# Performance work log

Measured on AMD Instinct MI355X. Metric: run time of the kernel, lower is better.

Reference implementation:

```python
import jax, jax.numpy as jnp
import numpy as np

B, N, D, H, L = 32, 576, 768, 8, 2
HD = D // H            # head_dim = 96
MLP = 4 * D            # 3072
GRID = 24              # sqrt(576), == max_positions
MP = 24                # max_positions
SD = 64                # spatial_dim
EPS = 1e-5


def _ln(x, g, b):
    m = jnp.mean(x, axis=-1, keepdims=True)
    v = jnp.mean((x - m) ** 2, axis=-1, keepdims=True)
    return (x - m) * jax.lax.rsqrt(v + EPS) * g + b


def setup_inputs() -> dict:
    key = jax.random.key(0)
    ks = jax.random.split(key, 16)
    s = 0.02
    inp = {
        "x": jax.random.normal(ks[0], (B, N, D), jnp.float32),
        # spatial position encoding params
        "row_embed": jax.random.normal(ks[1], (MP, SD // 2), jnp.float32) * s,
        "col_embed": jax.random.normal(ks[2], (MP, SD // 2), jnp.float32) * s,
        "pos_w": jax.random.normal(ks[3], (SD, D), jnp.float32) * s,
        "pos_b": jnp.zeros((D,), jnp.float32),
        "rel_bias": jax.random.normal(ks[4], (2 * MP - 1, 2 * MP - 1), jnp.float32) * s,
        # per-layer params, stacked on leading L axis
        "ln1_g": jnp.ones((L, D), jnp.float32),
        "ln1_b": jnp.zeros((L, D), jnp.float32),
        "ln2_g": jnp.ones((L, D), jnp.float32),
        "ln2_b": jnp.zeros((L, D), jnp.float32),
        "Wq": jax.random.normal(ks[5], (L, D, D), jnp.float32) * s,
        "bq": jnp.zeros((L, D), jnp.float32),
        "Wk": jax.random.normal(ks[6], (L, D, D), jnp.float32) * s,
        "bk": jnp.zeros((L, D), jnp.float32),
        "Wv": jax.random.normal(ks[7], (L, D, D), jnp.float32) * s,
        "bv": jnp.zeros((L, D), jnp.float32),
        "Wo": jax.random.normal(ks[8], (L, D, D), jnp.float32) * s,
        "bo": jnp.zeros((L, D), jnp.float32),
        "W1": jax.random.normal(ks[9], (L, D, MLP), jnp.float32) * s,
        "b1": jnp.zeros((L, MLP), jnp.float32),
        "W2": jax.random.normal(ks[10], (L, MLP, D), jnp.float32) * s,
        "b2": jnp.zeros((L, D), jnp.float32),
    }
    return inp


def reference(x, row_embed, col_embed, pos_w, pos_b, rel_bias,
              ln1_g, ln1_b, ln2_g, ln2_b,
              Wq, bq, Wk, bk, Wv, bv, Wo, bo,
              W1, b1, W2, b2):
    scale = HD ** -0.5

    # ---- absolute 2D position encoding (N = GRID*GRID, no CLS) ----
    pe = jnp.concatenate([
        jnp.broadcast_to(row_embed[:, None, :], (GRID, GRID, SD // 2)),
        jnp.broadcast_to(col_embed[None, :, :], (GRID, GRID, SD // 2)),
    ], axis=-1).reshape(N, SD)                      # [N, SD]
    x = x + (pe @ pos_w + pos_b)                    # broadcast over B

    # ---- relative position bias [N, N] ----
    coords = jnp.stack(jnp.meshgrid(jnp.arange(GRID), jnp.arange(GRID),
                                    indexing="ij")).reshape(2, N)  # [2, N]
    rel = coords[:, :, None] - coords[:, None, :]   # [2, N, N]
    idx = (rel[0] + MP - 1) * (2 * MP - 1) + (rel[1] + MP - 1)
    bias = rel_bias.reshape(-1)[idx]                # [N, N]

    # ---- reasoning layers ----
    for l in range(L):
        n1 = _ln(x, ln1_g[l], ln1_b[l])
        q = (n1 @ Wq[l] + bq[l]).reshape(B, N, H, HD)
        k = (n1 @ Wk[l] + bk[l]).reshape(B, N, H, HD)
        v = (n1 @ Wv[l] + bv[l]).reshape(B, N, H, HD)
        scores = jnp.einsum("bnhd,bmhd->bhnm", q, k) * scale + bias
        attn = jax.nn.softmax(scores, axis=-1)
        out = jnp.einsum("bhnm,bmhd->bnhd", attn, v).reshape(B, N, D)
        x = x + (out @ Wo[l] + bo[l])
        n2 = _ln(x, ln2_g[l], ln2_b[l])
        h = jax.nn.gelu(n2 @ W1[l] + b1[l], approximate=False)
        x = x + (h @ W2[l] + b2[l])
    return x
```

## Files before the change

kernel.cpp:

```cpp
#include <hip/hip_runtime.h>
#include <hip/hip_bf16.h>
#include <cstdint>
#include <cstddef>

typedef unsigned short u16;
using frag  = __attribute__((ext_vector_type(8))) short;
using f32x4 = __attribute__((ext_vector_type(4))) float;

#define DEV __device__ __forceinline__

DEV float bf2f(u16 u) { union { unsigned int i; float f; } x; x.i = ((unsigned int)u) << 16; return x.f; }
DEV u16 f2bf(float f) {
  union { float f; unsigned int i; } x; x.f = f;
  unsigned int r = x.i + 0x7fffu + ((x.i >> 16) & 1u);
  return (u16)(r >> 16);
}

#define MFMA16(a, b, c) __builtin_amdgcn_mfma_f32_16x16x32_bf16((a), (b), (c), 0, 0, 0)

DEV void cp16_g2l(const u16* g, u16* l) {
  __builtin_amdgcn_global_load_lds(
      reinterpret_cast<const __attribute__((address_space(1))) unsigned int*>(
          reinterpret_cast<uintptr_t>(g)),
      reinterpret_cast<__attribute__((address_space(3))) unsigned int*>(
          reinterpret_cast<uintptr_t>(l)),
      16, 0, 0);
}

template<int N> DEV void waitvm() {
  if constexpr (N == 0)      asm volatile("s_waitcnt vmcnt(0)" ::: "memory");
  else if constexpr (N == 3) asm volatile("s_waitcnt vmcnt(3)" ::: "memory");
  else if constexpr (N == 4) asm volatile("s_waitcnt vmcnt(4)" ::: "memory");
  else if constexpr (N == 6) asm volatile("s_waitcnt vmcnt(6)" ::: "memory");
  else if constexpr (N == 8) asm volatile("s_waitcnt vmcnt(8)" ::: "memory");
}

DEV void phase_barrier() {
  asm volatile("" ::: "memory");
  __builtin_amdgcn_sched_barrier(0);
  __builtin_amdgcn_s_barrier();
  __builtin_amdgcn_sched_barrier(0);
  asm volatile("" ::: "memory");
}

#define SB   32
#define SN   576
#define SD_  768
#define SH   8
#define SHD  96
#define SMLP 3072
#define BN_  (SB * SN)
#define IMG  (SN * SD_)
#define QKVS 2304

#define P_RE   0
#define P_CE   768
#define P_PW   1536
#define P_PB   50688
#define P_REL  51456
#define P_L1G  53696
#define P_L1B  55232
#define P_L2G  56768
#define P_L2B  58304
#define P_BQ   59840
#define P_BK   61376
#define P_BV   62912
#define P_BO   64448
#define P_B1   65984
#define P_B2   72128
#define P_FQB  73664
#define P_TOT  78272

__global__ void detect_kernel(const void* probe, int* flag) {
  if (threadIdx.x == 0 && blockIdx.x == 0) {
    unsigned int w = *(const unsigned int*)probe;
    flag[0] = (w == 0x3F800000u) ? 1 : 0;
  }
}

__global__ void canon_params(const void* re, const void* ce, const void* pw, const void* pb,
                             const void* rel, const void* l1g, const void* l1b,
                             const void* l2g, const void* l2b,
                             const void* pbq, const void* pbk, const void* pbv, const void* pbo,
                             const void* pb1, const void* pb2,
                             u16* __restrict__ P, const int* __restrict__ flag) {
  int i = blockIdx.x * 256 + threadIdx.x;
  const void* src; int si;
  if      (i < 768)     { src = re;  si = i; }
  else if (i < 1536)    { src = ce;  si = i - 768; }
  else if (i < 50688)   { src = pw;  si = i - 1536; }
  else if (i < 51456)   { src = pb;  si = i - 50688; }
  else if (i < 53665)   { src = rel; si = i - 51456; }
  else if (i < P_L1G)   { return; }
  else if (i < P_L1B)   { src = l1g; si = i - P_L1G; }
  else if (i < P_L2G)   { src = l1b; si = i - P_L1B; }
  else if (i < P_L2B)   { src = l2g; si = i - P_L2G; }
  else if (i < P_BQ)    { src = l2b; si = i - P_L2B; }
  else if (i < P_BK)    { src = pbq; si = i - P_BQ; }
  else if (i < P_BV)    { src = pbk; si = i - P_BK; }
  else if (i < P_BO)    { src = pbv; si = i - P_BV; }
  else if (i < P_B1)    { src = pbo; si = i - P_BO; }
  else if (i < P_B2)    { src = pb1; si = i - P_B1; }
  else if (i < P_FQB)   { src = pb2; si = i - P_B2; }
  else if (i < P_TOT) {
    int j = i - P_FQB, l = j / 2304, c = j % 2304;
    src = (c < 768) ? pbq : (c < 1536 ? pbk : pbv);
    si = l * 768 + (c % 768);
  }
  else return;
  P[i] = flag[0] ? f2bf(((const float*)src)[si]) : ((const u16*)src)[si];
}

__global__ void posenc_kernel(const u16* __restrict__ P, float* __restrict__ pe) {
  int n = blockIdx.x;
  int r = n / 24, c = n % 24;
  const u16* re = P + P_RE;
  const u16* ce = P + P_CE;
  const u16* pw = P + P_PW;
  const u16* pb = P + P_PB;
  for (int d = threadIdx.x; d < SD_; d += 256) {
    float acc = bf2f(pb[d]);
    for (int s = 0; s < 32; ++s) {
      acc += bf2f(re[r * 32 + s]) * bf2f(pw[s * SD_ + d]);
      acc += bf2f(ce[c * 32 + s]) * bf2f(pw[(32 + s) * SD_ + d]);
    }
    pe[n * SD_ + d] = acc;
  }
}

__global__ void bias_kernel(const u16* __restrict__ P, float* __restrict__ biasT) {
  int i = blockIdx.x * 256 + threadIdx.x;
  if (i < SN * SN) {
    int qi = i / SN, kj = i % SN;
    int ri = qi / 24, ci = qi % 24, rj = kj / 24, cj = kj % 24;
    int idx = (ri - rj + 23) * 47 + (ci - cj + 23);
    biasT[i] = bf2f(P[P_REL + idx]);
  }
}

__global__ void xinit_kernel(const void* __restrict__ xin, const float* __restrict__ pe,
                             float* __restrict__ X, const int* __restrict__ flag) {
  int idx = (blockIdx.x * 256 + threadIdx.x) * 4;
  int b = blockIdx.y;
  float vx, vy, vz, vw;
  if (flag[0]) {
    float4 t = *(const float4*)((const float*)xin + (size_t)b * IMG + idx);
    vx = t.x; vy = t.y; vz = t.z; vw = t.w;
  } else {
    ushort4 t = *(const ushort4*)((const u16*)xin + (size_t)b * IMG + idx);
    vx = bf2f(t.x); vy = bf2f(t.y); vz = bf2f(t.z); vw = bf2f(t.w);
  }
  float4 p = *(const float4*)(pe + idx);
  float4 o;
  o.x = vx + p.x; o.y = vy + p.y; o.z = vz + p.z; o.w = vw + p.w;
  *(float4*)(X + (size_t)b * IMG + idx) = o;
}

__global__ void transpose_any(const void* __restrict__ W, size_t eOff,
                              u16* __restrict__ Wt, int K, int N,
                              const int* __restrict__ flag) {
  __shared__ u16 tile[64][65];
  const int fp32 = flag[0];
  int n0 = blockIdx.x * 64, k0 = blockIdx.y * 64;
  int tx = threadIdx.x, ty = threadIdx.y;
#pragma unroll
  for (int j = 0; j < 16; ++j) {
    int k = ty + 4 * j;
    size_t si = eOff + (size_t)(k0 + k) * N + n0 + tx;
    tile[k][tx] = fp32 ? f2bf(((const float*)W)[si]) : ((const u16*)W)[si];
  }
  __syncthreads();
#pragma unroll
  for (int j = 0; j < 16; ++j) {
    int n = ty + 4 * j;
    Wt[(size_t)(n0 + n) * K + k0 + tx] = tile[tx][n];
  }
}

__global__ __launch_bounds__(256) void ln_kernel(const float* __restrict__ X,
                                                 const u16* __restrict__ g,
                                                 const u16* __restrict__ bb,
                                                 u16* __restrict__ Outn) {
  int row = blockIdx.x * 4 + (threadIdx.x >> 6);
  int lane = threadIdx.x & 63;
  const float* xr = X + (size_t)row * SD_;
  float4 v[3];
  float s = 0.f, sq = 0.f;
#pragma unroll
  for (int i = 0; i < 3; ++i) {
    v[i] = *(const float4*)(xr + i * 256 + lane * 4);
    s += v[i].x + v[i].y + v[i].z + v[i].w;
    sq += v[i].x * v[i].x + v[i].y * v[i].y + v[i].z * v[i].z + v[i].w * v[i].w;
  }
#pragma unroll
  for (int o = 1; o < 64; o <<= 1) {
    s += __shfl_xor(s, o, 64);
    sq += __shfl_xor(sq, o, 64);
  }
  float mean = s * (1.0f / 768.0f);
  float var = sq * (1.0f / 768.0f) - mean * mean;
  float rstd = rsqrtf(fmaxf(var, 0.f) + 1e-5f);
  u16* orow = Outn + (size_t)row * SD_;
#pragma unroll
  for (int i = 0; i < 3; ++i) {
    int d = i * 256 + lane * 4;
    ushort4 gv = *(const ushort4*)(g + d);
    ushort4 bv = *(const ushort4*)(bb + d);
    ushort4 ov;
    ov.x = f2bf((v[i].x - mean) * rstd * bf2f(gv.x) + bf2f(bv.x));
    ov.y = f2bf((v[i].y - mean) * rstd * bf2f(gv.y) + bf2f(bv.y));
    ov.z = f2bf((v[i].z - mean) * rstd * bf2f(gv.z) + bf2f(bv.z));
    ov.w = f2bf((v[i].w - mean) * rstd * bf2f(gv.w) + bf2f(bv.w));
    *(ushort4*)(orow + d) = ov;
  }
}

template<int MREP, int MODE>
__global__ __launch_bounds__(512, 2) void gemm256(
    const u16* __restrict__ A, const u16* __restrict__ Bt,
    const u16* __restrict__ bias, u16* __restrict__ Out,
    float* __restrict__ Xres, int Ncols, int K) {
  constexpr int BM = MREP * 32;
  constexpr int ASLOT = BM * 32;
  constexpr int BSLOT = 256 * 32;
  constexpr int LPT = (BM == 256) ? 4 : 3;
  __shared__ __align__(1024) u16 sA[4 * ASLOT];
  __shared__ __align__(1024) u16 sB[4 * BSLOT];

  const int tid = threadIdx.x;
  const int lane = tid & 63;
  const int w = tid >> 6;
  const int wm = w >> 2, wn = w & 3;
  const int m16 = lane & 15, q4 = lane >> 4;
  const int bn = blockIdx.x, bm = blockIdx.y;
  const int nt = K >> 5;

  const int srow = tid >> 2;
  const int kcol = (((tid & 3) ^ ((tid >> 3) & 3)) << 3);
  const u16* Ag = A + (size_t)(bm * BM + srow) * K + kcol;
  const u16* Bg = Bt + (size_t)(bn * 256 + srow) * K + kcol;
  const size_t rstep = (size_t)128 * K;
  u16* const Adst = sA + tid * 8;
  u16* const Bdst = sB + tid * 8;

  const int xk = ((q4 ^ ((m16 >> 1) & 3)) << 4);
  const char* const aBase = (const char*)sA + (((wm * (BM / 2) + m16) << 6) + xk);
  const char* const bBase = (const char*)sB + (((wn * 64 + m16) << 6) + xk);

  f32x4 acc[MREP][4] = {};

  auto stage_a = [&](int t) {
    const int s = t & 3;
    cp16_g2l(Ag + (size_t)t * 32, Adst + s * ASLOT);
    if constexpr (BM == 256) cp16_g2l(Ag + (size_t)t * 32 + rstep, Adst + s * ASLOT + 4096);
  };
  auto stage_b = [&](int t) {
    const int s = t & 3;
    cp16_g2l(Bg + (size_t)t * 32, Bdst + s * BSLOT);
    cp16_g2l(Bg + (size_t)t * 32 + rstep, Bdst + s * BSLOT + 4096);
  };

  if (nt > 0) { stage_a(0); stage_b(0); }
  if (nt > 1) { stage_a(1); stage_b(1); }
  if (nt > 2) { stage_a(2); stage_b(2); }
  if (nt > 2) waitvm<2 * LPT>(); else waitvm<0>();
  phase_barrier();

  for (int t = 0; t < nt; ++t) {
    const int s = t & 3;
    const bool st = (t + 3) < nt;
    const char* const aS = aBase + s * (ASLOT * 2);
    const char* const bS = bBase + s * (BSLOT * 2);
    frag bf[4], af[4];
#pragma unroll
    for (int j = 0; j < 4; ++j) bf[j] = *(const frag*)(bS + j * 1024);
#pragma unroll
    for (int i = 0; i < 4; ++i) af[i] = *(const frag*)(aS + i * 1024);
    if (st) stage_a(t + 3);
    if constexpr (MREP == 4) {
      if (st) stage_b(t + 3);
      if (t < nt - 3) waitvm<6>();
      else if (t == nt - 3) waitvm<3>();
      else if (t == nt - 2) waitvm<0>();
    }
    phase_barrier();
    __builtin_amdgcn_s_setprio(1);
#pragma unroll
    for (int i = 0; i < 4; ++i)
#pragma unroll
      for (int j = 0; j < 4; ++j) acc[i][j] = MFMA16(af[i], bf[j], acc[i][j]);
    __builtin_amdgcn_s_setprio(0);
    if constexpr (MREP == 8) {
      frag a2[4];
#pragma unroll
      for (int i = 0; i < 4; ++i) a2[i] = *(const frag*)(aS + 4096 + i * 1024);
      if (st) stage_b(t + 3);
      if (t < nt - 3) waitvm<8>();
      else if (t == nt - 3) waitvm<4>();
      else if (t == nt - 2) waitvm<0>();
      phase_barrier();
      __builtin_amdgcn_s_setprio(1);
#pragma unroll
      for (int i = 0; i < 4; ++i)
#pragma unroll
        for (int j = 0; j < 4; ++j) acc[4 + i][j] = MFMA16(a2[i], bf[j], acc[4 + i][j]);
      __builtin_amdgcn_s_setprio(0);
    }
  }

  const int col0 = bn * 256 + wn * 64;
  float bcol[4];
#pragma unroll
  for (int j = 0; j < 4; ++j) bcol[j] = bf2f(bias[col0 + j * 16 + m16]);

  if constexpr (MODE == 2) {
#pragma unroll
    for (int i = 0; i < MREP; ++i) {
      const int row0 = bm * BM + wm * (BM / 2) + i * 16 + q4 * 4;
#pragma unroll
      for (int j = 0; j < 4; ++j)
#pragma unroll
        for (int r = 0; r < 4; ++r)
          Xres[(size_t)(row0 + r) * Ncols + col0 + j * 16 + m16] += acc[i][j][r] + bcol[j];
    }
  } else {
    __syncthreads();
    u16* const wls = sA + w * 2048;
    const int lr = lane >> 3, lc = (lane & 7) * 8;
#pragma unroll
    for (int i = 0; i < MREP; ++i) {
#pragma unroll
      for (int j = 0; j < 4; ++j)
#pragma unroll
        for (int r = 0; r < 4; ++r) {
          float v = acc[i][j][r] + bcol[j];
          if constexpr (MODE == 1) v = 0.5f * v * (1.0f + erff(v * 0.70710678118654752f));
          wls[(q4 * 4 + r) * 72 + j * 16 + m16] = f2bf(v);
        }
      asm volatile("s_waitcnt lgkmcnt(0)" ::: "memory");
      frag o0 = *(const frag*)(wls + lr * 72 + lc);
      frag o1 = *(const frag*)(wls + (lr + 8) * 72 + lc);
      const size_t gr0 = (size_t)(bm * BM + wm * (BM / 2) + i * 16 + lr);
      *(frag*)(Out + gr0 * Ncols + col0 + lc) = o0;
      *(frag*)(Out + (gr0 + 8) * Ncols + col0 + lc) = o1;
    }
  }
}

__global__ __launch_bounds__(256) void attn_flash(const u16* __restrict__ QKV,
                                                  const float* __restrict__ biasT,
                                                  u16* __restrict__ Out, int b0) {
  __shared__ __align__(16) u16 Ks[64 * 104];
  __shared__ __align__(16) u16 Vt[96 * 72];
  __shared__ __align__(16) u16 Ps[64 * 72];
  const int tid = threadIdx.x, lane = tid & 63, w = tid >> 6;
  const int m16 = lane & 15, q4 = lane >> 4;
  const int qt = blockIdx.x, h = blockIdx.y, bl = blockIdx.z;
  const int q0 = qt * 64;
  const int row0 = bl * SN;
  const float scale = 0.10206207261596575f;

  frag aq[3];
  {
    const u16* qptr = QKV + (size_t)(row0 + q0 + w * 16 + m16) * QKVS + h * SHD;
#pragma unroll
    for (int ks = 0; ks < 3; ++ks) aq[ks] = *(const frag*)(qptr + ks * 32 + q4 * 8);
  }

  f32x4 oacc[6] = {};
  float mrun[4], lrun[4];
#pragma unroll
  for (int r = 0; r < 4; ++r) { mrun[r] = -1e30f; lrun[r] = 0.f; }

  for (int kt = 0; kt < 9; ++kt) {
    __syncthreads();
    for (int c = tid; c < 768; c += 256) {
      int key = c / 12, off = (c % 12) * 8;
      *(uint4*)(Ks + key * 104 + off) =
          *(const uint4*)(QKV + (size_t)(row0 + kt * 64 + key) * QKVS + 768 + h * SHD + off);
    }
    for (int c = tid; c < 768; c += 256) {
      int key = c / 12, off = (c % 12) * 8;
      uint4 u = *(const uint4*)(QKV + (size_t)(row0 + kt * 64 + key) * QKVS + 1536 + h * SHD + off);
      u16 tmp[8]; *(uint4*)tmp = u;
#pragma unroll
      for (int j = 0; j < 8; ++j) Vt[(off + j) * 72 + key] = tmp[j];
    }
    __syncthreads();

    f32x4 sa[4];
#pragma unroll
    for (int nt = 0; nt < 4; ++nt) {
      sa[nt] = (f32x4){0.f, 0.f, 0.f, 0.f};
#pragma unroll
      for (int ks = 0; ks < 3; ++ks) {
        frag bk = *(const frag*)(Ks + (nt * 16 + m16) * 104 + ks * 32 + q4 * 8);
        sa[nt] = MFMA16(aq[ks], bk, sa[nt]);
      }
    }

    float sv[4][4], mnew[4];
#pragma unroll
    for (int r = 0; r < 4; ++r) {
      int grow = q0 + w * 16 + q4 * 4 + r;
      const float* brow = biasT + (size_t)grow * SN + kt * 64;
      float mx = mrun[r];
#pragma unroll
      for (int nt = 0; nt < 4; ++nt) {
        float s = sa[nt][r] * scale + brow[nt * 16 + m16];
        sv[r][nt] = s;
        mx = fmaxf(mx, s);
      }
#pragma unroll
      for (int o = 1; o < 16; o <<= 1) mx = fmaxf(mx, __shfl_xor(mx, o, 64));
      mnew[r] = mx;
    }
#pragma unroll
    for (int r = 0; r < 4; ++r) {
      float alpha = __expf(mrun[r] - mnew[r]);
      mrun[r] = mnew[r];
      float psum = 0.f;
#pragma unroll
      for (int nt = 0; nt < 4; ++nt) {
        float p = __expf(sv[r][nt] - mnew[r]);
        psum += p;
        Ps[(w * 16 + q4 * 4 + r) * 72 + nt * 16 + m16] = f2bf(p);
      }
#pragma unroll
      for (int o = 1; o < 16; o <<= 1) psum += __shfl_xor(psum, o, 64);
      lrun[r] = lrun[r] * alpha + psum;
#pragma unroll
      for (int dt = 0; dt < 6; ++dt) oacc[dt][r] *= alpha;
    }
    __syncthreads();

#pragma unroll
    for (int ch = 0; ch < 2; ++ch) {
      frag ap = *(const frag*)(Ps + (w * 16 + m16) * 72 + ch * 32 + q4 * 8);
#pragma unroll
      for (int dt = 0; dt < 6; ++dt) {
        frag bv = *(const frag*)(Vt + (dt * 16 + m16) * 72 + ch * 32 + q4 * 8);
        oacc[dt] = MFMA16(ap, bv, oacc[dt]);
      }
    }
  }

#pragma unroll
  for (int r = 0; r < 4; ++r) {
    float inv = 1.0f / lrun[r];
    size_t obase = ((size_t)((b0 + bl) * SN + q0 + w * 16 + q4 * 4 + r)) * SD_ + h * SHD;
#pragma unroll
    for (int dt = 0; dt < 6; ++dt)
      Out[obase + dt * 16 + m16] = f2bf(oacc[dt][r] * inv);
  }
}

__global__ void castout_kernel(const float* __restrict__ X, void* __restrict__ out,
                               const int* __restrict__ flag) {
  int i = (blockIdx.x * 256 + threadIdx.x) * 4;
  float4 v = *(const float4*)(X + i);
  if (flag[0]) {
    *(float4*)((float*)out + i) = v;
  } else {
    ushort4 o;
    o.x = f2bf(v.x); o.y = f2bf(v.y); o.z = f2bf(v.z); o.w = f2bf(v.w);
    *(ushort4*)((u16*)out + i) = o;
  }
}

extern "C" void kernel_launch(void* const* d_in, const int* in_sizes, int n_in,
                              void* d_out, int out_size, void* d_ws, size_t ws_size,
                              hipStream_t stream) {
  const void* x_in      = d_in[0];
  const void* row_embed = d_in[1];
  const void* col_embed = d_in[2];
  const void* pos_w     = d_in[3];
  const void* pos_b     = d_in[4];
  const void* rel_bias  = d_in[5];
  const void* ln1_g = d_in[6];
  const void* ln1_b = d_in[7];
  const void* ln2_g = d_in[8];
  const void* ln2_b = d_in[9];
  const void* Wq = d_in[10];
  const void* bq = d_in[11];
  const void* Wk = d_in[12];
  const void* bk = d_in[13];
  const void* Wv = d_in[14];
  const void* bv = d_in[15];
  const void* Wo = d_in[16];
  const void* bo = d_in[17];
  const void* W1 = d_in[18];
  const void* b1 = d_in[19];
  const void* W2 = d_in[20];
  const void* b2 = d_in[21];

  const bool tierA = ws_size >= (size_t)131000000;
  const int BC = tierA ? 16 : 8;
  const int RC = tierA ? 9216 : 4608;
  const int mR = BC * SN;
  const size_t qkvB = (size_t)mR * QKVS * 2;
  size_t bigB = qkvB;
  { size_t hB = (size_t)RC * SMLP * 2; if (hB > bigB) bigB = hB; }

  char* ws = (char*)d_ws;
  size_t off = 0;
  auto alloc = [&](size_t bytes) -> void* {
    void* p = ws + off;
    off += (bytes + 255) & ~(size_t)255;
    return p;
  };

  int*   flag = (int*)alloc(256);
  float* X    = (float*)alloc((size_t)BN_ * SD_ * 4);
  char*  big  = (char*)alloc(bigB);
  u16* QKVc = (u16*)big;
  u16* Hbuf = (u16*)big;
  float* pe    = (float*)alloc((size_t)SN * SD_ * 4);
  float* biasT = (float*)alloc((size_t)SN * SN * 4);
  u16* P     = (u16*)alloc((size_t)P_TOT * 2 + 256);
  u16* WqkvT = (u16*)alloc((size_t)QKVS * SD_ * 2);
  u16* WoT   = (u16*)alloc((size_t)SD_ * SD_ * 2);
  u16* W1T   = (u16*)alloc((size_t)SD_ * SMLP * 2);
  u16* W2T   = (u16*)alloc((size_t)SMLP * SD_ * 2);
  u16* Nfull = (u16*)d_out;

  detect_kernel<<<1, 64, 0, stream>>>(ln1_g, flag);
  canon_params<<<(P_TOT + 255) / 256, 256, 0, stream>>>(
      row_embed, col_embed, pos_w, pos_b, rel_bias,
      ln1_g, ln1_b, ln2_g, ln2_b, bq, bk, bv, bo, b1, b2, P, flag);

  posenc_kernel<<<SN, 256, 0, stream>>>(P, pe);
  bias_kernel<<<(SN * SN + 255) / 256, 256, 0, stream>>>(P, biasT);
  xinit_kernel<<<dim3(IMG / 1024, SB), 256, 0, stream>>>(x_in, pe, X, flag);

  dim3 tb(64, 4);
  for (int l = 0; l < 2; ++l) {
    const size_t wOff = (size_t)l * SD_ * SD_;
    const size_t w1Off = (size_t)l * SD_ * SMLP;
    transpose_any<<<dim3(12, 12), tb, 0, stream>>>(Wq, wOff, WqkvT, SD_, SD_, flag);
    transpose_any<<<dim3(12, 12), tb, 0, stream>>>(Wk, wOff, WqkvT + SD_ * SD_, SD_, SD_, flag);
    transpose_any<<<dim3(12, 12), tb, 0, stream>>>(Wv, wOff, WqkvT + 2 * SD_ * SD_, SD_, SD_, flag);
    transpose_any<<<dim3(12, 12), tb, 0, stream>>>(Wo, wOff, WoT, SD_, SD_, flag);
    transpose_any<<<dim3(48, 12), tb, 0, stream>>>(W1, w1Off, W1T, SD_, SMLP, flag);
    transpose_any<<<dim3(12, 48), tb, 0, stream>>>(W2, w1Off, W2T, SMLP, SD_, flag);

    ln_kernel<<<BN_ / 4, 256, 0, stream>>>(X, P + P_L1G + l * SD_, P + P_L1B + l * SD_, Nfull);

    for (int c = 0; c < SB / BC; ++c) {
      const size_t r0 = (size_t)c * mR;
      gemm256<4, 0><<<dim3(QKVS / 256, mR / 128), 512, 0, stream>>>(
          Nfull + r0 * SD_, WqkvT, P + P_FQB + l * QKVS, QKVc, nullptr, QKVS, SD_);
      attn_flash<<<dim3(SN / 64, SH, BC), 256, 0, stream>>>(QKVc, biasT, Nfull, c * BC);
    }
    gemm256<4, 2><<<dim3(SD_ / 256, BN_ / 128), 512, 0, stream>>>(
        Nfull, WoT, P + P_BO + l * SD_, nullptr, X, SD_, SD_);

    ln_kernel<<<BN_ / 4, 256, 0, stream>>>(X, P + P_L2G + l * SD_, P + P_L2B + l * SD_, Nfull);

    for (int c = 0; c < BN_ / RC; ++c) {
      const size_t r0 = (size_t)c * RC;
      gemm256<8, 1><<<dim3(SMLP / 256, RC / 256), 512, 0, stream>>>(
          Nfull + r0 * SD_, W1T, P + P_B1 + l * SMLP, Hbuf, nullptr, SMLP, SD_);
      gemm256<4, 2><<<dim3(SD_ / 256, RC / 128), 512, 0, stream>>>(
          Hbuf, W2T, P + P_B2 + l * SD_, nullptr, X + r0 * SD_, SD_, SMLP);
    }
  }

  castout_kernel<<<(size_t)BN_ * SD_ / 1024, 256, 0, stream>>>(X, d_out, flag);
}
```

Measured before the change: 1.695 ms.

## Prefetch next K/V tile into registers and swizzle transposed V in LDS

The attention kernel now loads the next K/V tile from global memory into registers while the current tile is being computed, and writes it to LDS only after the PV MFMAs. Bias values are loaded into registers before the QK MFMAs, and s_setprio raises wave priority around the MFMA blocks. The transposed V buffer uses an XOR swizzle on the key index to reduce LDS bank conflicts on the scatter writes. It also drops the barrier between the Ps writes and the PV reads, since each wave reads only its own Ps rows, but it adds register pressure from the prefetch buffers.

```diff
diff --git a/kernel.cpp b/kernel.cpp
--- a/kernel.cpp
+++ b/kernel.cpp
@@ -360,6 +360,10 @@
   const int row0 = bl * SN;
   const float scale = 0.10206207261596575f;
 
+  int skey[3], soff[3];
+#pragma unroll
+  for (int u = 0; u < 3; ++u) { int c = tid + u * 256; skey[u] = c / 12; soff[u] = (c % 12) * 8; }
+
   frag aq[3];
   {
     const u16* qptr = QKV + (size_t)(row0 + q0 + w * 16 + m16) * QKVS + h * SHD;
@@ -372,23 +376,45 @@
 #pragma unroll
   for (int r = 0; r < 4; ++r) { mrun[r] = -1e30f; lrun[r] = 0.f; }
 
+  uint4 kreg[3], vreg[3];
+  auto loadKV = [&](int kt) {
+#pragma unroll
+    for (int u = 0; u < 3; ++u) {
+      const u16* base = QKV + (size_t)(row0 + kt * 64 + skey[u]) * QKVS + h * SHD + soff[u];
+      kreg[u] = *(const uint4*)(base + 768);
+      vreg[u] = *(const uint4*)(base + 1536);
+    }
+  };
+  auto writeKV = [&]() {
+#pragma unroll
+    for (int u = 0; u < 3; ++u) {
+      *(uint4*)(Ks + skey[u] * 104 + soff[u]) = kreg[u];
+      u16 tmp[8]; *(uint4*)tmp = vreg[u];
+#pragma unroll
+      for (int j = 0; j < 8; ++j) {
+        int d = soff[u] + j;
+        Vt[d * 72 + (skey[u] ^ (((d >> 3) & 7) << 3))] = tmp[j];
+      }
+    }
+  };
+
+  loadKV(0);
+  writeKV();
+  __syncthreads();
+
   for (int kt = 0; kt < 9; ++kt) {
-    __syncthreads();
-    for (int c = tid; c < 768; c += 256) {
-      int key = c / 12, off = (c % 12) * 8;
-      *(uint4*)(Ks + key * 104 + off) =
-          *(const uint4*)(QKV + (size_t)(row0 + kt * 64 + key) * QKVS + 768 + h * SHD + off);
-    }
-    for (int c = tid; c < 768; c += 256) {
-      int key = c / 12, off = (c % 12) * 8;
-      uint4 u = *(const uint4*)(QKV + (size_t)(row0 + kt * 64 + key) * QKVS + 1536 + h * SHD + off);
-      u16 tmp[8]; *(uint4*)tmp = u;
-#pragma unroll
-      for (int j = 0; j < 8; ++j) Vt[(off + j) * 72 + key] = tmp[j];
-    }
-    __syncthreads();
+    if (kt < 8) loadKV(kt + 1);
+
+    float breg[4][4];
+#pragma unroll
+    for (int r = 0; r < 4; ++r) {
+      const float* brow = biasT + (size_t)(q0 + w * 16 + q4 * 4 + r) * SN + kt * 64;
+#pragma unroll
+      for (int nt = 0; nt < 4; ++nt) breg[r][nt] = brow[nt * 16 + m16];
+    }
 
     f32x4 sa[4];
+    __builtin_amdgcn_s_setprio(1);
 #pragma unroll
     for (int nt = 0; nt < 4; ++nt) {
       sa[nt] = (f32x4){0.f, 0.f, 0.f, 0.f};
@@ -398,16 +424,15 @@
         sa[nt] = MFMA16(aq[ks], bk, sa[nt]);
       }
     }
+    __builtin_amdgcn_s_setprio(0);
 
     float sv[4][4], mnew[4];
 #pragma unroll
     for (int r = 0; r < 4; ++r) {
-      int grow = q0 + w * 16 + q4 * 4 + r;
-      const float* brow = biasT + (size_t)grow * SN + kt * 64;
       float mx = mrun[r];
 #pragma unroll
       for (int nt = 0; nt < 4; ++nt) {
-        float s = sa[nt][r] * scale + brow[nt * 16 + m16];
+        float s = sa[nt][r] * scale + breg[r][nt];
         sv[r][nt] = s;
         mx = fmaxf(mx, s);
       }
@@ -432,16 +457,24 @@
 #pragma unroll
       for (int dt = 0; dt < 6; ++dt) oacc[dt][r] *= alpha;
     }
-    __syncthreads();
-
+
+    __builtin_amdgcn_s_setprio(1);
 #pragma unroll
     for (int ch = 0; ch < 2; ++ch) {
       frag ap = *(const frag*)(Ps + (w * 16 + m16) * 72 + ch * 32 + q4 * 8);
 #pragma unroll
       for (int dt = 0; dt < 6; ++dt) {
-        frag bv = *(const frag*)(Vt + (dt * 16 + m16) * 72 + ch * 32 + q4 * 8);
+        const int d = dt * 16 + m16;
+        frag bv = *(const frag*)(Vt + d * 72 + ((ch * 32 + q4 * 8) ^ (((d >> 3) & 7) << 3)));
         oacc[dt] = MFMA16(ap, bv, oacc[dt]);
       }
+    }
+    __builtin_amdgcn_s_setprio(0);
+
+    if (kt < 8) {
+      __syncthreads();
+      writeKV();
+      __syncthreads();
     }
   }
 
```

Result: faster. 1.560 ms (-7.9%).
